# Performance work log

Measured on AMD Instinct MI355X. Metric: run time of the kernel, lower is better.

## Reference

```python
import jax, jax.numpy as jnp
import numpy as np

B, T, NIN = 128, 256, 16
H1 = H2 = 512
NACT = 4
SLOPE = 25.0  # snntorch FastSigmoid default slope

@jax.custom_vjp
def spike(x):
    return (x > 0).astype(x.dtype)

def _spike_fwd(x):
    return (x > 0).astype(x.dtype), x

def _spike_bwd(x, g):
    # FastSigmoid surrogate: d/dx = 1 / (slope*|x| + 1)^2
    return (g / (SLOPE * jnp.abs(x) + 1.0) ** 2,)

spike.defvjp(_spike_fwd, _spike_bwd)

def setup_inputs() -> dict:
    key = jax.random.key(0)
    ks = jax.random.split(key, 12)
    def lin(k, fan_in, shape):
        lim = 1.0 / np.sqrt(fan_in)
        return jax.random.uniform(k, shape, jnp.float32, -lim, lim)
    return {
        "batch": jax.random.uniform(ks[0], (B, T, NIN), jnp.float32, 0.0, 2.5),
        "W1": lin(ks[1], NIN, (H1, NIN)), "b1": lin(ks[2], NIN, (H1,)),
        "beta1": jax.random.uniform(ks[3], (H1,), jnp.float32),
        "thr1": jax.random.uniform(ks[4], (H1,), jnp.float32),
        "W2": lin(ks[5], H1, (H2, H1)), "b2": lin(ks[6], H1, (H2,)),
        "beta2": jax.random.uniform(ks[7], (H2,), jnp.float32),
        "thr2": jax.random.uniform(ks[8], (H2,), jnp.float32),
        "Wa": lin(ks[9], H2, (NACT, H2)), "ba": lin(ks[10], H2, (NACT,)),
        "beta_act": jnp.float32(0.95),
        "inp_min": jnp.float32(0.0),
        "inp_max": jnp.float32(2.5),
    }

def _lif_subtract(cur, mem, beta, thr):
    # snntorch Leaky: reset from PRE-update membrane, detached; subtract reset
    reset = jax.lax.stop_gradient((mem - thr > 0).astype(mem.dtype))
    mem = jnp.clip(beta, 0.0, 1.0) * mem + cur - reset * thr
    return spike(mem - thr), mem

def reference(batch, W1, b1, beta1, thr1, W2, b2, beta2, thr2, Wa, ba, beta_act, inp_min, inp_max):
    Bb = batch.shape[0]
    x_seq = jnp.swapaxes(batch, 0, 1)  # [T, B, NIN]
    mem1 = jnp.zeros((Bb, W1.shape[0]), batch.dtype)
    mem2 = jnp.zeros((Bb, W2.shape[0]), batch.dtype)
    mem_a = jnp.zeros((Bb, Wa.shape[0]), batch.dtype)

    def step(carry, x):
        mem1, mem2, mem_a = carry
        x = (x - inp_min) / (inp_max - inp_min)
        spk1, mem1 = _lif_subtract(x @ W1.T + b1, mem1, beta1, thr1)
        spk2, mem2 = _lif_subtract(spk1 @ W2.T + b2, mem2, beta2, thr2)
        act = spk2 @ Wa.T + ba
        # action_lif: reset_mechanism='none', beta=0.95 learnable
        mem_a = jnp.clip(beta_act, 0.0, 1.0) * mem_a + act
        return (mem1, mem2, mem_a), mem_a.reshape(-1)  # torch: mem_act.reshape((1,-1))

    _, vals = jax.lax.scan(step, (mem1, mem2, mem_a), x_seq)
    # torch.stack(values, dim=1) of (1, B*NACT) tensors -> (1, T, B*NACT)
    return vals[None, :, :]
```

## Files before the change

### kernel.cpp

```cpp
#include <hip/hip_runtime.h>
#include <stdint.h>

typedef __attribute__((ext_vector_type(8))) short short8;
typedef __attribute__((ext_vector_type(4))) float f32x4;

#define T_STEPS 256
#define BATCH   128

#define LDS_BARRIER() asm volatile("s_waitcnt lgkmcnt(0)\n\ts_barrier" ::: "memory")

static __device__ inline unsigned short f2bf(float f) {
    unsigned int u = __float_as_uint(f);
    unsigned int r = u + 0x7FFFu + ((u >> 16) & 1u);
    return (unsigned short)(r >> 16);
}
static __device__ inline unsigned pack_hi16(unsigned a, unsigned b) {
    return (a >> 16) | (b & 0xFFFF0000u);
}

__global__ __launch_bounds__(256) void k_prep(
    const float* __restrict__ W2, const float* __restrict__ W1,
    const float* __restrict__ b1, const float* __restrict__ thr1,
    const float* __restrict__ imin_p, const float* __restrict__ imax_p,
    const float* __restrict__ batch,
    unsigned short* __restrict__ W2hi, unsigned short* __restrict__ W2lo,
    unsigned short* __restrict__ W1rows, float* __restrict__ b1s,
    unsigned short* __restrict__ Xf)
{
    int blk = blockIdx.x, tid = threadIdx.x;
    if (blk < 256) {
        int gid = blk * 256 + tid;
        f32x4 wv = *(const f32x4*)(W2 + (size_t)gid * 4);
        unsigned short hi[4], lo[4];
#pragma unroll
        for (int e = 0; e < 4; ++e) {
            float wf = wv[e];
            unsigned short h = f2bf(wf);
            float hf = __uint_as_float(((unsigned int)h) << 16);
            hi[e] = h;
            lo[e] = f2bf(wf - hf);
        }
        uint2 ph, pl;
        ph.x = (unsigned)hi[0] | ((unsigned)hi[1] << 16);
        ph.y = (unsigned)hi[2] | ((unsigned)hi[3] << 16);
        pl.x = (unsigned)lo[0] | ((unsigned)lo[1] << 16);
        pl.y = (unsigned)lo[2] | ((unsigned)lo[3] << 16);
        *(uint2*)(W2hi + (size_t)gid * 4) = ph;
        *(uint2*)(W2lo + (size_t)gid * 4) = pl;
    } else if (blk < 258) {
        int h = (blk - 256) * 256 + tid;
        float wsc = 1.0f / thr1[h];
        unsigned short row[64];
#pragma unroll
        for (int k = 0; k < 16; ++k) {
            float wv = W1[h * 16 + k] * wsc;
            unsigned a = __float_as_uint(wv) & 0xFFFF0000u;
            float r1 = wv - __uint_as_float(a);
            unsigned m = __float_as_uint(r1) & 0xFFFF0000u;
            float r2 = r1 - __uint_as_float(m);
            unsigned l = __float_as_uint(r2) & 0xFFFF0000u;
            row[k]      = (unsigned short)(a >> 16);
            row[16 + k] = (unsigned short)(m >> 16);
            row[32 + k] = (unsigned short)(l >> 16);
            row[48 + k] = 0;
        }
        b1s[h] = b1[h] * wsc;
        uint4* dst = (uint4*)(W1rows + (size_t)h * 64);
#pragma unroll
        for (int i = 0; i < 8; ++i) dst[i] = ((uint4*)row)[i];
    } else {
        int gid   = (blk - 258) * 256 + tid;
        int lane  = gid & 63;
        int btile = (gid >> 6) & 7;
        int t     = gid >> 9;
        int q     = lane >> 4, m15 = lane & 15;
        int b     = btile * 16 + m15;
        float imin = imin_p[0];
        float isc  = 1.0f / (imax_p[0] - imin);
        const float* xp = batch + ((size_t)b * T_STEPS + t) * 16 + (q & 1) * 8;
        unsigned uh[8], um[8], ul[8];
#pragma unroll
        for (int j = 0; j < 8; ++j) {
            float xv = (xp[j] - imin) * isc;
            unsigned a = __float_as_uint(xv) & 0xFFFF0000u;
            float r1 = xv - __uint_as_float(a);
            unsigned m = __float_as_uint(r1) & 0xFFFF0000u;
            float r2 = r1 - __uint_as_float(m);
            unsigned l = __float_as_uint(r2) & 0xFFFF0000u;
            uh[j] = a; um[j] = m; ul[j] = l;
        }
        uint4 B1, B2, XL;
        B1.x = pack_hi16(uh[0], uh[1]); B1.y = pack_hi16(uh[2], uh[3]);
        B1.z = pack_hi16(uh[4], uh[5]); B1.w = pack_hi16(uh[6], uh[7]);
        B2.x = pack_hi16(um[0], um[1]); B2.y = pack_hi16(um[2], um[3]);
        B2.z = pack_hi16(um[4], um[5]); B2.w = pack_hi16(um[6], um[7]);
        XL.x = pack_hi16(ul[0], ul[1]); XL.y = pack_hi16(ul[2], ul[3]);
        XL.z = pack_hi16(ul[4], ul[5]); XL.w = pack_hi16(ul[6], ul[7]);
        uint4 B3 = (q < 2) ? XL : B1;
        unsigned short* dst = Xf + (((size_t)t * 8 + btile) * 3) * 512 + lane * 8;
        *(uint4*)(dst +    0) = B1;
        *(uint4*)(dst +  512) = B2;
        *(uint4*)(dst + 1024) = B3;
    }
}

__global__ __launch_bounds__(1024, 4) void k_main(
    const unsigned short* __restrict__ Xf,
    const unsigned short* __restrict__ W2hi, const unsigned short* __restrict__ W2lo,
    const unsigned short* __restrict__ W1rows, const float* __restrict__ b1s,
    const float* __restrict__ beta1, const float* __restrict__ b2,
    const float* __restrict__ beta2, const float* __restrict__ thr2,
    unsigned short* __restrict__ spkbits)
{
    __shared__ unsigned short Aw[8192];
    __shared__ float Cbuf[2][4096];

    int tid  = threadIdx.x;
    int lane = tid & 63;
    int w    = tid >> 6;
    int q    = lane >> 4, m15 = lane & 15;
    int btile = blockIdx.x & 7;
    int slice = blockIdx.x >> 3;
    int rr = w & 3, qi = w >> 2;

    short8 A1[2], A2[2];
#pragma unroll
    for (int c = 0; c < 2; ++c) {
        const unsigned short* rp = W1rows + (size_t)(w * 32 + c * 16 + m15) * 64;
        A1[c] = *(const short8*)(rp + q * 8);
        A2[c] = *(const short8*)(rp + q * 8 + (q >> 1) * 16);
    }
    int jg = slice * 16 + m15;
    short8 bhi = *(const short8*)(W2hi + (size_t)jg * 512 + w * 32 + q * 8);
    short8 blo = *(const short8*)(W2lo + (size_t)jg * 512 + w * 32 + q * 8);

    f32x4 b14[2], bet1[2];
#pragma unroll
    for (int c = 0; c < 2; ++c) {
        int h0 = w * 32 + c * 16 + q * 4;
        b14[c] = *(const f32x4*)(b1s + h0);
        f32x4 bb = *(const f32x4*)(beta1 + h0);
#pragma unroll
        for (int r = 0; r < 4; ++r) bet1[c][r] = fminf(fmaxf(bb[r], 0.0f), 1.0f);
    }
    float m1[8], spk1f[8];
#pragma unroll
    for (int i = 0; i < 8; ++i) { m1[i] = 0.0f; spk1f[i] = 0.0f; }

    float beta2r = fminf(fmaxf(beta2[jg], 0.0f), 1.0f);
    float thr2r  = thr2[jg];
    float nthr2  = -thr2r;
    float b2r    = b2[jg];
    float m2 = 0.0f, spk2f = 0.0f;

    const unsigned short* xbase = Xf + ((size_t)btile * 3) * 512 + lane * 8;
    const unsigned short* xpA = xbase + 2 * 12288;
    const unsigned short* xpB = xbase + 3 * 12288;
    uint4 xP[3], xQ[3];
#pragma unroll
    for (int f = 0; f < 3; ++f) xP[f] = *(const uint4*)(xbase + f * 512);
#pragma unroll
    for (int f = 0; f < 3; ++f) xQ[f] = *(const uint4*)(xbase + 12288 + f * 512);

    unsigned short* awp = Aw + w * 512;
    int wr0 = ((q >> 1)) * 128 + (m15 ^ (q >> 1)) * 8 + (q & 1) * 4;
    int wr1 = wr0 + 256;
    int rdo = (q * 16 + (m15 ^ (q & 1))) * 8;
    int sidx = w * 64 + (lane ^ (qi * 16));
    int ridx = rr * 1024 + q * 256 + ((qi ^ q) * 16 + m15);

    unsigned short* spkp = spkbits + ((size_t)btile * 16 + (qi * 4 + rr)) * 32 + slice;

    auto gemm1 = [&](uint4* x, f32x4* D) __attribute__((always_inline)) {
        union { uint4 u; short8 s; } B0, B1, B2;
        B0.u = x[0]; B1.u = x[1]; B2.u = x[2];
#pragma unroll
        for (int c = 0; c < 2; ++c) {
            D[c] = b14[c];
            D[c] = __builtin_amdgcn_mfma_f32_16x16x32_bf16(A1[c], B0.s, D[c], 0, 0, 0);
            D[c] = __builtin_amdgcn_mfma_f32_16x16x32_bf16(A1[c], B1.s, D[c], 0, 0, 0);
            D[c] = __builtin_amdgcn_mfma_f32_16x16x32_bf16(A2[c], B2.s, D[c], 0, 0, 0);
        }
    };
    auto lifpack = [&](f32x4* D) __attribute__((always_inline)) {
#pragma unroll
        for (int i = 0; i < 8; ++i) {
            int c = i >> 2, r = i & 3;
            float mv = fmaf(bet1[c][r], m1[i], D[c][r]);
            mv -= spk1f[i];
            bool sp = mv > 1.0f;
            m1[i] = mv;
            spk1f[i] = sp ? 1.0f : 0.0f;
        }
        uint2 pk0, pk1;
        pk0.x = pack_hi16(__float_as_uint(spk1f[0]), __float_as_uint(spk1f[1]));
        pk0.y = pack_hi16(__float_as_uint(spk1f[2]), __float_as_uint(spk1f[3]));
        pk1.x = pack_hi16(__float_as_uint(spk1f[4]), __float_as_uint(spk1f[5]));
        pk1.y = pack_hi16(__float_as_uint(spk1f[6]), __float_as_uint(spk1f[7]));
        *(uint2*)(awp + wr0) = pk0;
        *(uint2*)(awp + wr1) = pk1;
    };
    auto rtail = [&](float s0, float s1, float s2, float s3) __attribute__((always_inline)) {
        float s = (s0 + s1) + (s2 + s3);
        s += __shfl_xor(s, 16, 64);
        s += __shfl_xor(s, 32, 64);
        m2 = fmaf(beta2r, m2, b2r + s);
        m2 = fmaf(spk2f, nthr2, m2);
        bool sp2 = m2 > thr2r;
        spk2f = sp2 ? 1.0f : 0.0f;
        unsigned long long mask = __ballot(sp2);
        if (lane == 0) *spkp = (unsigned short)(mask & 0xFFFFu);
        spkp += BATCH * 32;
    };
    auto g2sc = [&](float* cb) __attribute__((always_inline)) {
        union { uint4 u; short8 s; } af;
        af.u = *(uint4*)(awp + rdo);
        f32x4 C2 = { 0.f, 0.f, 0.f, 0.f };
        C2 = __builtin_amdgcn_mfma_f32_16x16x32_bf16(af.s, bhi, C2, 0, 0, 0);
        C2 = __builtin_amdgcn_mfma_f32_16x16x32_bf16(af.s, blo, C2, 0, 0, 0);
        cb[sidx]        = C2[0];
        cb[sidx + 1024] = C2[1];
        cb[sidx + 2048] = C2[2];
        cb[sidx + 3072] = C2[3];
    };

    f32x4 D0[2], D1[2];
    gemm1(xP, D0);

#pragma unroll 1
    for (int i = 0; i < T_STEPS; i += 2) {
        {
            const float* rb = Cbuf[1];
            float s0 = rb[ridx], s1 = rb[ridx + 64], s2 = rb[ridx + 128], s3 = rb[ridx + 192];
            lifpack(D0);
#pragma unroll
            for (int f = 0; f < 3; ++f) xP[f] = *(const uint4*)(xpA + f * 512);
            xpA += 24576;
            gemm1(xQ, D1);
            if (i) rtail(s0, s1, s2, s3);
            g2sc(Cbuf[0]);
        }
        LDS_BARRIER();
        {
            const float* rb = Cbuf[0];
            float s0 = rb[ridx], s1 = rb[ridx + 64], s2 = rb[ridx + 128], s3 = rb[ridx + 192];
            lifpack(D1);
#pragma unroll
            for (int f = 0; f < 3; ++f) xQ[f] = *(const uint4*)(xpB + f * 512);
            xpB += 24576;
            gemm1(xP, D0);
            rtail(s0, s1, s2, s3);
            g2sc(Cbuf[1]);
        }
        LDS_BARRIER();
    }
    {
        const float* rb = Cbuf[1];
        float s0 = rb[ridx], s1 = rb[ridx + 64], s2 = rb[ridx + 128], s3 = rb[ridx + 192];
        rtail(s0, s1, s2, s3);
    }
}

__global__ __launch_bounds__(256) void k_act(
    const unsigned short* __restrict__ spkbits,
    const float* __restrict__ Wa, const float* __restrict__ ba,
    const float* __restrict__ beta_act_p, float* __restrict__ out)
{
    __shared__ f32x4 waT[512];
    __shared__ f32x4 sc[256];
    int tid = threadIdx.x;
    int b   = blockIdx.x;

    for (int j = tid; j < 512; j += 256) {
        f32x4 v = { Wa[j], Wa[512 + j], Wa[1024 + j], Wa[1536 + j] };
        waT[j] = v;
    }
    float bact = fminf(fmaxf(beta_act_p[0], 0.0f), 1.0f);
    f32x4 acc = { ba[0], ba[1], ba[2], ba[3] };
    __syncthreads();

    const unsigned short* sp = spkbits + ((size_t)tid * BATCH + b) * 32;
    unsigned int wbuf[16];
#pragma unroll
    for (int r = 0; r < 4; ++r) {
        uint4 v = *(const uint4*)(sp + r * 8);
        wbuf[r*4+0] = v.x; wbuf[r*4+1] = v.y; wbuf[r*4+2] = v.z; wbuf[r*4+3] = v.w;
    }
    for (int s = 0; s < 32; ++s) {
        unsigned int wd = (wbuf[s >> 1] >> ((s & 1) * 16)) & 0xFFFFu;
#pragma unroll
        for (int i = 0; i < 16; ++i) {
            float sel = ((wd >> i) & 1u) ? 1.0f : 0.0f;
            f32x4 wv = waT[s * 16 + i];
            acc[0] = fmaf(sel, wv[0], acc[0]);
            acc[1] = fmaf(sel, wv[1], acc[1]);
            acc[2] = fmaf(sel, wv[2], acc[2]);
            acc[3] = fmaf(sel, wv[3], acc[3]);
        }
    }
    sc[tid] = acc;
    __syncthreads();
    float bd = bact;
    for (int d = 1; d < 256; d <<= 1) {
        f32x4 cv = sc[tid];
        f32x4 pv = { 0.f, 0.f, 0.f, 0.f };
        if (tid >= d) pv = sc[tid - d];
        __syncthreads();
        cv[0] = fmaf(bd, pv[0], cv[0]);
        cv[1] = fmaf(bd, pv[1], cv[1]);
        cv[2] = fmaf(bd, pv[2], cv[2]);
        cv[3] = fmaf(bd, pv[3], cv[3]);
        sc[tid] = cv;
        __syncthreads();
        bd *= bd;
    }
    f32x4 res = sc[tid];
    *(f32x4*)(out + (size_t)tid * 512 + b * 4) = res;
}

extern "C" void kernel_launch(void* const* d_in, const int* in_sizes, int n_in,
                              void* d_out, int out_size, void* d_ws, size_t ws_size,
                              hipStream_t stream)
{
    const float* batch    = (const float*)d_in[0];
    const float* W1       = (const float*)d_in[1];
    const float* b1       = (const float*)d_in[2];
    const float* beta1    = (const float*)d_in[3];
    const float* thr1     = (const float*)d_in[4];
    const float* W2       = (const float*)d_in[5];
    const float* b2       = (const float*)d_in[6];
    const float* beta2    = (const float*)d_in[7];
    const float* thr2     = (const float*)d_in[8];
    const float* Wa       = (const float*)d_in[9];
    const float* ba       = (const float*)d_in[10];
    const float* beta_act = (const float*)d_in[11];
    const float* inp_min  = (const float*)d_in[12];
    const float* inp_max  = (const float*)d_in[13];
    float* out            = (float*)d_out;

    char* ws = (char*)d_ws;
    unsigned short* W2hi    = (unsigned short*)ws;
    unsigned short* W2lo    = (unsigned short*)(ws + (512u << 10));
    unsigned short* W1rows  = (unsigned short*)(ws + (1u << 20));
    float*          b1s     = (float*)(ws + (1u << 20) + (64u << 10));
    unsigned short* Xf      = (unsigned short*)(ws + (2u << 20));
    unsigned short* spkbits = (unsigned short*)(ws + (8u << 20));

    hipLaunchKernelGGL(k_prep, dim3(770), dim3(256), 0, stream,
                       W2, W1, b1, thr1, inp_min, inp_max, batch,
                       W2hi, W2lo, W1rows, b1s, Xf);
    hipLaunchKernelGGL(k_main, dim3(256), dim3(1024), 0, stream,
                       Xf, W2hi, W2lo, W1rows, b1s, beta1, b2, beta2, thr2, spkbits);
    hipLaunchKernelGGL(k_act, dim3(128), dim3(256), 0, stream, spkbits, Wa, ba, beta_act, out);
}
```

Before: 308.7 us.

## Distribute layer-1 LIF across blocks and exchange spike bits via global flags

Before, every block recomputed the full 512-neuron layer-1 GEMM and LIF for its batch tile. Now each block's wave 0 computes only its 16-neuron slice of layer 1 and publishes the spike bitmask to global memory, tagged with a 0x5555 flag. All waves spin on volatile loads until all slices for the timestep arrive, then build the layer-2 A operand from the bits. This removes redundant layer-1 work and the LDS spike staging, but adds a cross-block dependency on global-memory polling each step. That relies on all 256 blocks being co-resident and risks stalls from the global round-trip latency.

```diff
diff --git a/kernel.cpp b/kernel.cpp
--- a/kernel.cpp
+++ b/kernel.cpp
@@ -25,7 +25,7 @@
     const float* __restrict__ batch,
     unsigned short* __restrict__ W2hi, unsigned short* __restrict__ W2lo,
     unsigned short* __restrict__ W1rows, float* __restrict__ b1s,
-    unsigned short* __restrict__ Xf)
+    unsigned short* __restrict__ Xf, unsigned* __restrict__ spkglob)
 {
     int blk = blockIdx.x, tid = threadIdx.x;
     if (blk < 256) {
@@ -68,7 +68,7 @@
         uint4* dst = (uint4*)(W1rows + (size_t)h * 64);
 #pragma unroll
         for (int i = 0; i < 8; ++i) dst[i] = ((uint4*)row)[i];
-    } else {
+    } else if (blk < 770) {
         int gid   = (blk - 258) * 256 + tid;
         int lane  = gid & 63;
         int btile = (gid >> 6) & 7;
@@ -101,6 +101,12 @@
         *(uint4*)(dst +    0) = B1;
         *(uint4*)(dst +  512) = B2;
         *(uint4*)(dst + 1024) = B3;
+    } else {
+        int pb = blk - 770;
+        unsigned* dst = spkglob + ((size_t)pb * 256 + tid) * 16;
+        uint4 P = { 0xAAAAAAAAu, 0xAAAAAAAAu, 0xAAAAAAAAu, 0xAAAAAAAAu };
+#pragma unroll
+        for (int i = 0; i < 4; ++i) *(uint4*)(dst + i * 4) = P;
     }
 }
 
@@ -110,9 +116,8 @@
     const unsigned short* __restrict__ W1rows, const float* __restrict__ b1s,
     const float* __restrict__ beta1, const float* __restrict__ b2,
     const float* __restrict__ beta2, const float* __restrict__ thr2,
-    unsigned short* __restrict__ spkbits)
+    unsigned* __restrict__ spkglob, unsigned short* __restrict__ spkbits)
 {
-    __shared__ unsigned short Aw[8192];
     __shared__ float Cbuf[2][4096];
 
     int tid  = threadIdx.x;
@@ -123,29 +128,9 @@
     int slice = blockIdx.x >> 3;
     int rr = w & 3, qi = w >> 2;
 
-    short8 A1[2], A2[2];
-#pragma unroll
-    for (int c = 0; c < 2; ++c) {
-        const unsigned short* rp = W1rows + (size_t)(w * 32 + c * 16 + m15) * 64;
-        A1[c] = *(const short8*)(rp + q * 8);
-        A2[c] = *(const short8*)(rp + q * 8 + (q >> 1) * 16);
-    }
     int jg = slice * 16 + m15;
     short8 bhi = *(const short8*)(W2hi + (size_t)jg * 512 + w * 32 + q * 8);
     short8 blo = *(const short8*)(W2lo + (size_t)jg * 512 + w * 32 + q * 8);
-
-    f32x4 b14[2], bet1[2];
-#pragma unroll
-    for (int c = 0; c < 2; ++c) {
-        int h0 = w * 32 + c * 16 + q * 4;
-        b14[c] = *(const f32x4*)(b1s + h0);
-        f32x4 bb = *(const f32x4*)(beta1 + h0);
-#pragma unroll
-        for (int r = 0; r < 4; ++r) bet1[c][r] = fminf(fmaxf(bb[r], 0.0f), 1.0f);
-    }
-    float m1[8], spk1f[8];
-#pragma unroll
-    for (int i = 0; i < 8; ++i) { m1[i] = 0.0f; spk1f[i] = 0.0f; }
 
     float beta2r = fminf(fmaxf(beta2[jg], 0.0f), 1.0f);
     float thr2r  = thr2[jg];
@@ -153,54 +138,89 @@
     float b2r    = b2[jg];
     float m2 = 0.0f, spk2f = 0.0f;
 
-    const unsigned short* xbase = Xf + ((size_t)btile * 3) * 512 + lane * 8;
-    const unsigned short* xpA = xbase + 2 * 12288;
-    const unsigned short* xpB = xbase + 3 * 12288;
-    uint4 xP[3], xQ[3];
-#pragma unroll
-    for (int f = 0; f < 3; ++f) xP[f] = *(const uint4*)(xbase + f * 512);
-#pragma unroll
-    for (int f = 0; f < 3; ++f) xQ[f] = *(const uint4*)(xbase + 12288 + f * 512);
-
-    unsigned short* awp = Aw + w * 512;
-    int wr0 = ((q >> 1)) * 128 + (m15 ^ (q >> 1)) * 8 + (q & 1) * 4;
-    int wr1 = wr0 + 256;
-    int rdo = (q * 16 + (m15 ^ (q & 1))) * 8;
     int sidx = w * 64 + (lane ^ (qi * 16));
     int ridx = rr * 1024 + q * 256 + ((qi ^ q) * 16 + m15);
-
     unsigned short* spkp = spkbits + ((size_t)btile * 16 + (qi * 4 + rr)) * 32 + slice;
 
-    auto gemm1 = [&](uint4* x, f32x4* D) __attribute__((always_inline)) {
+    const unsigned short* rp = W1rows + (size_t)(slice * 16 + m15) * 64;
+    short8 A1p = *(const short8*)(rp + q * 8);
+    short8 A2p = *(const short8*)(rp + q * 8 + (q >> 1) * 16);
+    int h0p = slice * 16 + q * 4;
+    f32x4 b14p = *(const f32x4*)(b1s + h0p);
+    f32x4 bet1p;
+    {
+        f32x4 bb = *(const f32x4*)(beta1 + h0p);
+#pragma unroll
+        for (int r = 0; r < 4; ++r) bet1p[r] = fminf(fmaxf(bb[r], 0.0f), 1.0f);
+    }
+    float m1p[4] = { 0.f, 0.f, 0.f, 0.f }, sp1p[4] = { 0.f, 0.f, 0.f, 0.f };
+
+    const unsigned short* xbase = Xf + ((size_t)btile * 3) * 512 + lane * 8;
+    unsigned* pstore = spkglob + (size_t)btile * 512 + slice * 16 + lane;
+    const unsigned* cbase = spkglob + (size_t)btile * 512 + w * 32 + q * 8;
+
+    uint4 x0[3];
+
+    auto ldx = [&](int t) __attribute__((always_inline)) {
+        int tn = (t < T_STEPS) ? t : T_STEPS - 1;
+        const unsigned short* xp = xbase + (size_t)tn * 12288;
+#pragma unroll
+        for (int f = 0; f < 3; ++f) x0[f] = *(const uint4*)(xp + f * 512);
+    };
+    auto produce = [&](int t) __attribute__((always_inline)) {
         union { uint4 u; short8 s; } B0, B1, B2;
-        B0.u = x[0]; B1.u = x[1]; B2.u = x[2];
-#pragma unroll
-        for (int c = 0; c < 2; ++c) {
-            D[c] = b14[c];
-            D[c] = __builtin_amdgcn_mfma_f32_16x16x32_bf16(A1[c], B0.s, D[c], 0, 0, 0);
-            D[c] = __builtin_amdgcn_mfma_f32_16x16x32_bf16(A1[c], B1.s, D[c], 0, 0, 0);
-            D[c] = __builtin_amdgcn_mfma_f32_16x16x32_bf16(A2[c], B2.s, D[c], 0, 0, 0);
-        }
-    };
-    auto lifpack = [&](f32x4* D) __attribute__((always_inline)) {
-#pragma unroll
-        for (int i = 0; i < 8; ++i) {
-            int c = i >> 2, r = i & 3;
-            float mv = fmaf(bet1[c][r], m1[i], D[c][r]);
-            mv -= spk1f[i];
+        B0.u = x0[0]; B1.u = x0[1]; B2.u = x0[2];
+        f32x4 D = b14p;
+        D = __builtin_amdgcn_mfma_f32_16x16x32_bf16(A1p, B0.s, D, 0, 0, 0);
+        D = __builtin_amdgcn_mfma_f32_16x16x32_bf16(A1p, B1.s, D, 0, 0, 0);
+        D = __builtin_amdgcn_mfma_f32_16x16x32_bf16(A2p, B2.s, D, 0, 0, 0);
+        unsigned long long mk[4];
+#pragma unroll
+        for (int r = 0; r < 4; ++r) {
+            float mv = fmaf(bet1p[r], m1p[r], D[r]);
+            mv -= sp1p[r];
             bool sp = mv > 1.0f;
-            m1[i] = mv;
-            spk1f[i] = sp ? 1.0f : 0.0f;
-        }
-        uint2 pk0, pk1;
-        pk0.x = pack_hi16(__float_as_uint(spk1f[0]), __float_as_uint(spk1f[1]));
-        pk0.y = pack_hi16(__float_as_uint(spk1f[2]), __float_as_uint(spk1f[3]));
-        pk1.x = pack_hi16(__float_as_uint(spk1f[4]), __float_as_uint(spk1f[5]));
-        pk1.y = pack_hi16(__float_as_uint(spk1f[6]), __float_as_uint(spk1f[7]));
-        *(uint2*)(awp + wr0) = pk0;
-        *(uint2*)(awp + wr1) = pk1;
-    };
-    auto rtail = [&](float s0, float s1, float s2, float s3) __attribute__((always_inline)) {
+            m1p[r] = mv;
+            sp1p[r] = sp ? 1.0f : 0.0f;
+            mk[r] = __ballot(sp);
+        }
+        if (lane < 16) {
+            int rs = lane & 3, qs = lane >> 2;
+            unsigned long long mv_ = mk[0];
+            mv_ = (rs == 1) ? mk[1] : mv_;
+            mv_ = (rs == 2) ? mk[2] : mv_;
+            mv_ = (rs == 3) ? mk[3] : mv_;
+            unsigned dw  = (qs & 2) ? (unsigned)(mv_ >> 32) : (unsigned)mv_;
+            unsigned v16 = (qs & 1) ? (dw >> 16) : (dw & 0xFFFFu);
+            *(volatile unsigned*)(pstore + (size_t)t * 4096) = v16 | 0x55550000u;
+        }
+    };
+    auto cload = [&](int t, uint4& a, uint4& b) __attribute__((always_inline)) {
+        volatile const unsigned* p = cbase + (size_t)t * 4096;
+        a.x = p[0]; a.y = p[1]; a.z = p[2]; a.w = p[3];
+        b.x = p[4]; b.y = p[5]; b.z = p[6]; b.w = p[7];
+    };
+    auto consume = [&](int t, uint4 a, uint4 b, float* cb) __attribute__((always_inline)) {
+        while (true) {
+            unsigned acc = a.x & a.y & a.z & a.w & b.x & b.y & b.z & b.w;
+            if (__all((acc >> 16) == 0x5555u)) break;
+            cload(t, a, b);
+        }
+        union { unsigned u[4]; short8 s; } af;
+        af.u[0] = (((a.x >> m15) & 1) ? 0x3F80u : 0u) | (((a.y >> m15) & 1) ? 0x3F800000u : 0u);
+        af.u[1] = (((a.z >> m15) & 1) ? 0x3F80u : 0u) | (((a.w >> m15) & 1) ? 0x3F800000u : 0u);
+        af.u[2] = (((b.x >> m15) & 1) ? 0x3F80u : 0u) | (((b.y >> m15) & 1) ? 0x3F800000u : 0u);
+        af.u[3] = (((b.z >> m15) & 1) ? 0x3F80u : 0u) | (((b.w >> m15) & 1) ? 0x3F800000u : 0u);
+        f32x4 C2 = { 0.f, 0.f, 0.f, 0.f };
+        C2 = __builtin_amdgcn_mfma_f32_16x16x32_bf16(af.s, bhi, C2, 0, 0, 0);
+        C2 = __builtin_amdgcn_mfma_f32_16x16x32_bf16(af.s, blo, C2, 0, 0, 0);
+        cb[sidx]        = C2[0];
+        cb[sidx + 1024] = C2[1];
+        cb[sidx + 2048] = C2[2];
+        cb[sidx + 3072] = C2[3];
+    };
+    auto rtail = [&](const float* cb) __attribute__((always_inline)) {
+        float s0 = cb[ridx], s1 = cb[ridx + 64], s2 = cb[ridx + 128], s3 = cb[ridx + 192];
         float s = (s0 + s1) + (s2 + s3);
         s += __shfl_xor(s, 16, 64);
         s += __shfl_xor(s, 32, 64);
@@ -212,52 +232,27 @@
         if (lane == 0) *spkp = (unsigned short)(mask & 0xFFFFu);
         spkp += BATCH * 32;
     };
-    auto g2sc = [&](float* cb) __attribute__((always_inline)) {
-        union { uint4 u; short8 s; } af;
-        af.u = *(uint4*)(awp + rdo);
-        f32x4 C2 = { 0.f, 0.f, 0.f, 0.f };
-        C2 = __builtin_amdgcn_mfma_f32_16x16x32_bf16(af.s, bhi, C2, 0, 0, 0);
-        C2 = __builtin_amdgcn_mfma_f32_16x16x32_bf16(af.s, blo, C2, 0, 0, 0);
-        cb[sidx]        = C2[0];
-        cb[sidx + 1024] = C2[1];
-        cb[sidx + 2048] = C2[2];
-        cb[sidx + 3072] = C2[3];
-    };
-
-    f32x4 D0[2], D1[2];
-    gemm1(xP, D0);
+
+    if (w == 0) {
+        ldx(0); produce(0);
+        ldx(1); produce(1);
+        ldx(2);
+    }
+    uint4 cA0, cA1, cB0, cB1;
+    cload(0, cA0, cA1);
 
 #pragma unroll 1
-    for (int i = 0; i < T_STEPS; i += 2) {
-        {
-            const float* rb = Cbuf[1];
-            float s0 = rb[ridx], s1 = rb[ridx + 64], s2 = rb[ridx + 128], s3 = rb[ridx + 192];
-            lifpack(D0);
-#pragma unroll
-            for (int f = 0; f < 3; ++f) xP[f] = *(const uint4*)(xpA + f * 512);
-            xpA += 24576;
-            gemm1(xQ, D1);
-            if (i) rtail(s0, s1, s2, s3);
-            g2sc(Cbuf[0]);
-        }
+    for (int t = 0; t < T_STEPS; t += 2) {
+        cload(t + 1, cB0, cB1);
+        if (w == 0) { produce(t + 2); ldx(t + 3); }
+        consume(t, cA0, cA1, Cbuf[0]);
         LDS_BARRIER();
-        {
-            const float* rb = Cbuf[0];
-            float s0 = rb[ridx], s1 = rb[ridx + 64], s2 = rb[ridx + 128], s3 = rb[ridx + 192];
-            lifpack(D1);
-#pragma unroll
-            for (int f = 0; f < 3; ++f) xQ[f] = *(const uint4*)(xpB + f * 512);
-            xpB += 24576;
-            gemm1(xP, D0);
-            rtail(s0, s1, s2, s3);
-            g2sc(Cbuf[1]);
-        }
+        rtail(Cbuf[0]);
+        cload(t + 2, cA0, cA1);
+        if (w == 0) { produce(t + 3); ldx(t + 4); }
+        consume(t + 1, cB0, cB1, Cbuf[1]);
         LDS_BARRIER();
-    }
-    {
-        const float* rb = Cbuf[1];
-        float s0 = rb[ridx], s1 = rb[ridx + 64], s2 = rb[ridx + 128], s3 = rb[ridx + 192];
-        rtail(s0, s1, s2, s3);
+        rtail(Cbuf[1]);
     }
 }
 
@@ -345,11 +340,12 @@
     float*          b1s     = (float*)(ws + (1u << 20) + (64u << 10));
     unsigned short* Xf      = (unsigned short*)(ws + (2u << 20));
     unsigned short* spkbits = (unsigned short*)(ws + (8u << 20));
-
-    hipLaunchKernelGGL(k_prep, dim3(770), dim3(256), 0, stream,
+    unsigned*       spkglob = (unsigned*)(ws + (10u << 20));
+
+    hipLaunchKernelGGL(k_prep, dim3(1028), dim3(256), 0, stream,
                        W2, W1, b1, thr1, inp_min, inp_max, batch,
-                       W2hi, W2lo, W1rows, b1s, Xf);
+                       W2hi, W2lo, W1rows, b1s, Xf, spkglob);
     hipLaunchKernelGGL(k_main, dim3(256), dim3(1024), 0, stream,
-                       Xf, W2hi, W2lo, W1rows, b1s, beta1, b2, beta2, thr2, spkbits);
+                       Xf, W2hi, W2lo, W1rows, b1s, beta1, b2, beta2, thr2, spkglob, spkbits);
     hipLaunchKernelGGL(k_act, dim3(128), dim3(256), 0, stream, spkbits, Wa, ba, beta_act, out);
 }
```

Result: slower. 521.9 us (+69.0%).
